# Performance work log

Hardware: AMD Instinct MI355X
Metric: run time of the kernel (lower is better)

## Reference

```python
import jax, jax.numpy as jnp
import numpy as np

N_NODES = 100000
N_EDGES = 1600000
D_IN = 128
D_OUT = 128
EPS = 1e-5


def setup_inputs() -> dict:
    key = jax.random.key(0)
    ks = jax.random.split(key, 5)
    x = jax.random.normal(ks[0], (N_NODES, D_IN), dtype=jnp.float32)
    edge_index = jax.random.randint(ks[1], (2, N_EDGES), 0, N_NODES, dtype=jnp.int64)
    scale = 1.0 / np.sqrt(D_IN)
    W_root = jax.random.normal(ks[2], (D_IN, D_OUT), dtype=jnp.float32) * scale
    W_rel = jax.random.normal(ks[3], (D_IN, D_OUT), dtype=jnp.float32) * scale
    b_rel = jax.random.normal(ks[4], (D_OUT,), dtype=jnp.float32) * 0.01
    gamma = jnp.ones((D_OUT,), dtype=jnp.float32)
    beta = jnp.zeros((D_OUT,), dtype=jnp.float32)
    return {"x": x, "edge_index": edge_index, "W_root": W_root, "W_rel": W_rel,
            "b_rel": b_rel, "gamma": gamma, "beta": beta}


def reference(x, edge_index, W_root, W_rel, b_rel, gamma, beta):
    # GraphConv: out = aggr(x_j) @ W_rel + b_rel + x @ W_root   (aggr = sum)
    src = edge_index[0]
    dst = edge_index[1]
    aggr = jax.ops.segment_sum(x[src], dst, num_segments=x.shape[0])  # [N, D_IN]
    h = aggr @ W_rel + b_rel + x @ W_root                              # [N, D_OUT]
    # NodeLevelBatchNorm (training mode: batch stats over node dim, biased var)
    mean = jnp.mean(h, axis=0)
    var = jnp.mean(jnp.square(h - mean), axis=0)
    h_norm = (h - mean) * jax.lax.rsqrt(var + EPS) * gamma + beta
    return jax.nn.relu(h_norm)
```

## Files before the change

kernel.cpp:

```cpp
#include <hip/hip_runtime.h>

#define N_NODES 100000
#define N_EDGES 1600000
#define D 128
#define NB 196
#define EPT 10
#define CHUNK 2560
#define BIN_BLOCKS 625
#define CVT_X_BLOCKS 6250
#define ZROW N_NODES

typedef __bf16 bf16x8 __attribute__((ext_vector_type(8)));
typedef float f32x4 __attribute__((ext_vector_type(4)));

__device__ __forceinline__ unsigned f2bf(float f) {
    unsigned u = __float_as_uint(f);
    return (u + 0x7fffu + ((u >> 16) & 1u)) >> 16;
}
__device__ __forceinline__ float bf_lo(unsigned u) { return __uint_as_float(u << 16); }
__device__ __forceinline__ float bf_hi(unsigned u) { return __uint_as_float(u & 0xffff0000u); }

__global__ __launch_bounds__(256) void prep_kernel(const float* __restrict__ x,
                                                   const float* __restrict__ Wrel,
                                                   const float* __restrict__ Wroot,
                                                   const int* __restrict__ ei,
                                                   unsigned short* __restrict__ x_bf,
                                                   unsigned short* __restrict__ Wt,
                                                   int* __restrict__ bcount) {
    __shared__ int h[256];
    int b = blockIdx.x;
    int t = threadIdx.x;
    if (b < CVT_X_BLOCKS) {
        size_t i = ((size_t)b * 256 + t) * 8;
        float4 v0 = *(const float4*)(x + i);
        float4 v1 = *(const float4*)(x + i + 4);
        uint4 p;
        p.x = f2bf(v0.x) | (f2bf(v0.y) << 16);
        p.y = f2bf(v0.z) | (f2bf(v0.w) << 16);
        p.z = f2bf(v1.x) | (f2bf(v1.y) << 16);
        p.w = f2bf(v1.z) | (f2bf(v1.w) << 16);
        *(uint4*)(x_bf + i) = p;
    } else if (b < CVT_X_BLOCKS + 128) {
        int c = b - CVT_X_BLOCKS;
        float v = (t < 128) ? Wrel[t * D + c] : Wroot[(t - 128) * D + c];
        Wt[c * 256 + t] = (unsigned short)f2bf(v);
    } else if (b == CVT_X_BLOCKS + 128) {
        if (t < 16) *(uint4*)(x_bf + (size_t)ZROW * D + t * 8) = make_uint4(0, 0, 0, 0);
    } else {
        int blk = b - (CVT_X_BLOCKS + 129);
        h[t] = 0;
        __syncthreads();
        int base = blk * CHUNK;
#pragma unroll
        for (int i = 0; i < EPT; ++i) {
            int dst = ei[N_EDGES + base + i * 256 + t];
            atomicAdd(&h[dst >> 9], 1);
        }
        __syncthreads();
        if (t < NB && h[t]) atomicAdd(&bcount[t], h[t]);
    }
}

__global__ __launch_bounds__(256) void bscan_kernel(const int* __restrict__ bcount,
                                                    int* __restrict__ bucket_base,
                                                    int* __restrict__ bcur) {
    __shared__ int s[256];
    int t = threadIdx.x;
    int v = (t < NB) ? bcount[t] : 0;
    s[t] = v;
    __syncthreads();
    for (int off = 1; off < 256; off <<= 1) {
        int a = (t >= off) ? s[t - off] : 0;
        __syncthreads();
        s[t] += a;
        __syncthreads();
    }
    int excl = s[t] - v;
    if (t < NB) {
        bucket_base[t] = excl;
        bcur[t] = excl;
    }
    if (t == NB) bucket_base[NB] = N_EDGES;
}

__global__ __launch_bounds__(256) void binify_kernel(const int* __restrict__ ei,
                                                     int* __restrict__ bcur,
                                                     unsigned* __restrict__ epk) {
    __shared__ int lhist[256];
    __shared__ int lstart[256];
    __shared__ int lfill[256];
    __shared__ int gbase[256];
    __shared__ uint2 stage[CHUNK];

    int t = threadIdx.x;
    int base = blockIdx.x * CHUNK;
    lhist[t] = 0;
    lfill[t] = 0;
    __syncthreads();

    int src[EPT], dst[EPT];
#pragma unroll
    for (int i = 0; i < EPT; ++i) {
        int e = base + i * 256 + t;
        src[i] = ei[e];
        dst[i] = ei[N_EDGES + e];
        atomicAdd(&lhist[dst[i] >> 9], 1);
    }
    __syncthreads();

    int v = lhist[t];
    lstart[t] = v;
    __syncthreads();
    for (int off = 1; off < 256; off <<= 1) {
        int a = (t >= off) ? lstart[t - off] : 0;
        __syncthreads();
        lstart[t] += a;
        __syncthreads();
    }
    int excl = lstart[t] - v;
    if (t < NB && v > 0) gbase[t] = atomicAdd(&bcur[t], v);
    __syncthreads();
    lstart[t] = excl;
    __syncthreads();

#pragma unroll
    for (int i = 0; i < EPT; ++i) {
        int b = dst[i] >> 9;
        int lp = atomicAdd(&lfill[b], 1);
        stage[lstart[b] + lp] = make_uint2((unsigned)src[i], (unsigned)dst[i]);
    }
    __syncthreads();

    for (int i = t; i < CHUNK; i += 256) {
        uint2 p = stage[i];
        int b = (int)(p.y >> 9);
        unsigned code = p.x | ((p.y & 511u) << 17);
        epk[gbase[b] + (i - lstart[b])] = code;
    }
}

__global__ __launch_bounds__(256) void place_kernel(const unsigned* __restrict__ epk,
                                                    const int* __restrict__ bucket_base,
                                                    int* __restrict__ rowstart,
                                                    int* __restrict__ srcs) {
    __shared__ int bufA[512];
    __shared__ int bufB[512];
    int b = blockIdx.x;
    int t = threadIdx.x;
    int pbeg = bucket_base[b];
    int pend = bucket_base[b + 1];

    bufA[t] = 0;
    bufA[t + 256] = 0;
    __syncthreads();
    for (int i = pbeg + t; i < pend; i += 256)
        atomicAdd(&bufA[epk[i] >> 17], 1);
    __syncthreads();

    for (int j = t; j < 512; j += 256) bufB[j] = j ? bufA[j - 1] : 0;
    __syncthreads();
    int* cur = bufB;
    int* nxt = bufA;
    for (int off = 1; off < 512; off <<= 1) {
        for (int j = t; j < 512; j += 256)
            nxt[j] = cur[j] + ((j >= off) ? cur[j - off] : 0);
        __syncthreads();
        int* tmp = cur; cur = nxt; nxt = tmp;
    }

    for (int j = t; j < 512; j += 256) {
        int gnode = (b << 9) + j;
        int val = pbeg + cur[j];
        if (gnode <= N_NODES) rowstart[gnode] = val;
        nxt[j] = val;
    }
    __syncthreads();

    for (int i = pbeg + t; i < pend; i += 256) {
        unsigned code = epk[i];
        int pos = atomicAdd(&nxt[code >> 17], 1);
        srcs[pos] = (int)(code & 0x1FFFFu);
    }
}

__global__ __launch_bounds__(256) void gather_kernel(const unsigned short* __restrict__ x_bf,
                                                     const int* __restrict__ rowstart,
                                                     const int* __restrict__ srcs,
                                                     unsigned short* __restrict__ aggr_bf) {
    int t = threadIdx.x;
    int node = blockIdx.x * 16 + (t >> 4);
    int l16 = t & 15;
    int begin = rowstart[node];
    int end = rowstart[node + 1];
    const unsigned short* xp = x_bf + l16 * 8;
    float a0 = 0.f, a1 = 0.f, a2 = 0.f, a3 = 0.f;
    float a4 = 0.f, a5 = 0.f, a6 = 0.f, a7 = 0.f;
    for (int e = begin; e < end; e += 8) {
        int idx[8];
#pragma unroll
        for (int i = 0; i < 8; ++i) {
            int ee = e + i;
            int ec = (ee < end) ? ee : (end - 1);
            int sv = srcs[ec];
            idx[i] = (ee < end) ? sv : ZROW;
        }
        uint4 u[8];
#pragma unroll
        for (int i = 0; i < 8; ++i) u[i] = *(const uint4*)(xp + (size_t)idx[i] * D);
#pragma unroll
        for (int i = 0; i < 8; ++i) {
            a0 += bf_lo(u[i].x);
            a1 += bf_hi(u[i].x);
            a2 += bf_lo(u[i].y);
            a3 += bf_hi(u[i].y);
            a4 += bf_lo(u[i].z);
            a5 += bf_hi(u[i].z);
            a6 += bf_lo(u[i].w);
            a7 += bf_hi(u[i].w);
        }
    }
    uint4 w;
    w.x = f2bf(a0) | (f2bf(a1) << 16);
    w.y = f2bf(a2) | (f2bf(a3) << 16);
    w.z = f2bf(a4) | (f2bf(a5) << 16);
    w.w = f2bf(a6) | (f2bf(a7) << 16);
    *(uint4*)(aggr_bf + (size_t)node * D + l16 * 8) = w;
}

#define LDSTRIDE 40
__global__ __launch_bounds__(256) void gemm_mfma(const unsigned short* __restrict__ aggr_bf,
                                                 const unsigned short* __restrict__ x_bf,
                                                 const unsigned short* __restrict__ Wt,
                                                 const float* __restrict__ brel,
                                                 unsigned short* __restrict__ h_bf,
                                                 float* __restrict__ gsum,
                                                 float* __restrict__ gss) {
    __shared__ unsigned short As[128][LDSTRIDE];
    __shared__ unsigned short Bs[128][LDSTRIDE];
    __shared__ float sbias[128];
    __shared__ float SredS[4][128];
    __shared__ float SredQ[4][128];

    const int t = threadIdx.x;
    const int wave = t >> 6;
    const int lane = t & 63;
    const int quad = lane >> 4;
    const int l16 = lane & 15;
    const int blockRow = blockIdx.x * 128;

    if (t < 128) sbias[t] = brel[t];

    f32x4 acc[2][8];
#pragma unroll
    for (int i = 0; i < 2; ++i)
#pragma unroll
        for (int j = 0; j < 8; ++j) acc[i][j] = (f32x4){0.f, 0.f, 0.f, 0.f};

    for (int kc = 0; kc < 8; ++kc) {
        const unsigned short* Asrc = (kc < 4) ? aggr_bf : x_bf;
        const int k0 = (kc & 3) * 32;
#pragma unroll
        for (int s = t; s < 512; s += 256) {
            int row = s >> 2;
            int q = (s & 3) * 8;
            int grow = blockRow + row;
            uint4 v = make_uint4(0, 0, 0, 0);
            if (grow < N_NODES) v = *(const uint4*)(Asrc + (size_t)grow * D + k0 + q);
            *(uint4*)&As[row][q] = v;
        }
#pragma unroll
        for (int s = t; s < 512; s += 256) {
            int col = s >> 2;
            int q = (s & 3) * 8;
            uint4 v = *(const uint4*)(Wt + col * 256 + kc * 32 + q);
            *(uint4*)&Bs[col][q] = v;
        }
        __syncthreads();

        bf16x8 afrag0 = *(bf16x8*)&As[wave * 32 + l16][quad * 8];
        bf16x8 afrag1 = *(bf16x8*)&As[wave * 32 + 16 + l16][quad * 8];
#pragma unroll
        for (int ct = 0; ct < 8; ++ct) {
            bf16x8 bfrag = *(bf16x8*)&Bs[ct * 16 + l16][quad * 8];
            acc[0][ct] = __builtin_amdgcn_mfma_f32_16x16x32_bf16(afrag0, bfrag, acc[0][ct], 0, 0, 0);
            acc[1][ct] = __builtin_amdgcn_mfma_f32_16x16x32_bf16(afrag1, bfrag, acc[1][ct], 0, 0, 0);
        }
        __syncthreads();
    }

    float csum[8], css[8];
#pragma unroll
    for (int ct = 0; ct < 8; ++ct) { csum[ct] = 0.f; css[ct] = 0.f; }

#pragma unroll
    for (int rt = 0; rt < 2; ++rt) {
#pragma unroll
        for (int ct = 0; ct < 8; ++ct) {
            int col = ct * 16 + l16;
            float bv = sbias[col];
#pragma unroll
            for (int reg = 0; reg < 4; ++reg) {
                int row = blockRow + wave * 32 + rt * 16 + quad * 4 + reg;
                if (row < N_NODES) {
                    float v = acc[rt][ct][reg] + bv;
                    h_bf[(size_t)row * D + col] = (unsigned short)f2bf(v);
                    csum[ct] += v;
                    css[ct] += v * v;
                }
            }
        }
    }
#pragma unroll
    for (int ct = 0; ct < 8; ++ct) {
        float s = csum[ct], q = css[ct];
        s += __shfl_xor(s, 16);
        s += __shfl_xor(s, 32);
        q += __shfl_xor(q, 16);
        q += __shfl_xor(q, 32);
        if (quad == 0) {
            SredS[wave][ct * 16 + l16] = s;
            SredQ[wave][ct * 16 + l16] = q;
        }
    }
    __syncthreads();
    if (t < 128) {
        float s = SredS[0][t] + SredS[1][t] + SredS[2][t] + SredS[3][t];
        float q = SredQ[0][t] + SredQ[1][t] + SredQ[2][t] + SredQ[3][t];
        unsafeAtomicAdd(&gsum[t], s);
        unsafeAtomicAdd(&gss[t], q);
    }
}

__global__ __launch_bounds__(256) void norm_kernel(const unsigned short* __restrict__ h_bf,
                                                   float* __restrict__ out,
                                                   const float* __restrict__ gsum,
                                                   const float* __restrict__ gss,
                                                   const float* __restrict__ gamma,
                                                   const float* __restrict__ beta) {
    __shared__ float sscale[128];
    __shared__ float sshift[128];
    int t = threadIdx.x;
    if (t < 128) {
        const float inv_n = 1.0f / (float)N_NODES;
        float mean = gsum[t] * inv_n;
        float var = gss[t] * inv_n - mean * mean;
        float rs = rsqrtf(var + 1e-5f);
        float sc = gamma[t] * rs;
        sscale[t] = sc;
        sshift[t] = beta[t] - mean * sc;
    }
    __syncthreads();
    size_t e = ((size_t)blockIdx.x * 256 + t) * 4;
    if (e >= (size_t)N_NODES * D) return;
    int c = (int)(e & 127);
    uint2 u = *(const uint2*)(h_bf + e);
    float4 v;
    v.x = fmaxf(bf_lo(u.x) * sscale[c + 0] + sshift[c + 0], 0.f);
    v.y = fmaxf(bf_hi(u.x) * sscale[c + 1] + sshift[c + 1], 0.f);
    v.z = fmaxf(bf_lo(u.y) * sscale[c + 2] + sshift[c + 2], 0.f);
    v.w = fmaxf(bf_hi(u.y) * sscale[c + 3] + sshift[c + 3], 0.f);
    *(float4*)(out + e) = v;
}

extern "C" void kernel_launch(void* const* d_in, const int* in_sizes, int n_in,
                              void* d_out, int out_size, void* d_ws, size_t ws_size,
                              hipStream_t stream) {
    const float* x     = (const float*)d_in[0];
    const int*   ei    = (const int*)d_in[1];
    const float* Wroot = (const float*)d_in[2];
    const float* Wrel  = (const float*)d_in[3];
    const float* brel  = (const float*)d_in[4];
    const float* gamma = (const float*)d_in[5];
    const float* beta  = (const float*)d_in[6];
    float* out = (float*)d_out;

    unsigned short* aggr_bf = (unsigned short*)d_ws;
    unsigned short* x_bf    = aggr_bf + (size_t)N_NODES * D;
    unsigned short* Wt      = x_bf + (size_t)(N_NODES + 1) * D;
    float* gsum  = (float*)(Wt + 128 * 256);
    float* gss   = gsum + 128;
    int* bcount  = (int*)(gss + 128);
    int* bucket_base = bcount + 256;
    int* bcur    = bucket_base + 256;
    int* rowstart = bcur + 256;
    unsigned* epk = (unsigned*)(rowstart + 100352);
    int* srcs    = (int*)(epk + N_EDGES);
    unsigned short* h_bf = (unsigned short*)epk;

    hipMemsetAsync(gsum, 0, 512 * sizeof(int), stream);

    prep_kernel<<<CVT_X_BLOCKS + 129 + BIN_BLOCKS, 256, 0, stream>>>(
        x, Wrel, Wroot, ei, x_bf, Wt, bcount);
    bscan_kernel<<<1, 256, 0, stream>>>(bcount, bucket_base, bcur);
    binify_kernel<<<BIN_BLOCKS, 256, 0, stream>>>(ei, bcur, epk);
    place_kernel<<<NB, 256, 0, stream>>>(epk, bucket_base, rowstart, srcs);
    gather_kernel<<<N_NODES / 16, 256, 0, stream>>>(x_bf, rowstart, srcs, aggr_bf);
    gemm_mfma<<<(N_NODES + 127) / 128, 256, 0, stream>>>(aggr_bf, x_bf, Wt, brel, h_bf, gsum, gss);
    norm_kernel<<<12500, 256, 0, stream>>>(h_bf, out, gsum, gss, gamma, beta);
}
```

Measured before the change: 287.8 us.

## Load GEMM A fragments directly from global and stage W in fragment order

The MFMA GEMM no longer stages A tiles through LDS. Each wave reads its bf16x8 A fragments straight from global memory. The weight matrix is copied into LDS once per half (aggregate part, then root part) in MFMA-fragment order, so each lane reads its B fragment contiguously. This cuts the number of block barriers from 16 to 3 and removes the padded-stride LDS traffic for A. In exchange, A loads are no longer coalesced through shared memory, and the row-bounds check on A reads is gone, so the last block reads past N_NODES unless the buffers are padded.

```diff
diff --git a/kernel.cpp b/kernel.cpp
--- a/kernel.cpp
+++ b/kernel.cpp
@@ -227,7 +227,6 @@
     *(uint4*)(aggr_bf + (size_t)node * D + l16 * 8) = w;
 }
 
-#define LDSTRIDE 40
 __global__ __launch_bounds__(256) void gemm_mfma(const unsigned short* __restrict__ aggr_bf,
                                                  const unsigned short* __restrict__ x_bf,
                                                  const unsigned short* __restrict__ Wt,
@@ -235,8 +234,7 @@
                                                  unsigned short* __restrict__ h_bf,
                                                  float* __restrict__ gsum,
                                                  float* __restrict__ gss) {
-    __shared__ unsigned short As[128][LDSTRIDE];
-    __shared__ unsigned short Bs[128][LDSTRIDE];
+    __shared__ unsigned short Bf[2048 * 8];
     __shared__ float sbias[128];
     __shared__ float SredS[4][128];
     __shared__ float SredQ[4][128];
@@ -256,36 +254,35 @@
 #pragma unroll
         for (int j = 0; j < 8; ++j) acc[i][j] = (f32x4){0.f, 0.f, 0.f, 0.f};
 
-    for (int kc = 0; kc < 8; ++kc) {
-        const unsigned short* Asrc = (kc < 4) ? aggr_bf : x_bf;
-        const int k0 = (kc & 3) * 32;
-#pragma unroll
-        for (int s = t; s < 512; s += 256) {
-            int row = s >> 2;
-            int q = (s & 3) * 8;
-            int grow = blockRow + row;
-            uint4 v = make_uint4(0, 0, 0, 0);
-            if (grow < N_NODES) v = *(const uint4*)(Asrc + (size_t)grow * D + k0 + q);
-            *(uint4*)&As[row][q] = v;
-        }
-#pragma unroll
-        for (int s = t; s < 512; s += 256) {
-            int col = s >> 2;
-            int q = (s & 3) * 8;
-            uint4 v = *(const uint4*)(Wt + col * 256 + kc * 32 + q);
-            *(uint4*)&Bs[col][q] = v;
-        }
-        __syncthreads();
-
-        bf16x8 afrag0 = *(bf16x8*)&As[wave * 32 + l16][quad * 8];
-        bf16x8 afrag1 = *(bf16x8*)&As[wave * 32 + 16 + l16][quad * 8];
-#pragma unroll
-        for (int ct = 0; ct < 8; ++ct) {
-            bf16x8 bfrag = *(bf16x8*)&Bs[ct * 16 + l16][quad * 8];
-            acc[0][ct] = __builtin_amdgcn_mfma_f32_16x16x32_bf16(afrag0, bfrag, acc[0][ct], 0, 0, 0);
-            acc[1][ct] = __builtin_amdgcn_mfma_f32_16x16x32_bf16(afrag1, bfrag, acc[1][ct], 0, 0, 0);
-        }
-        __syncthreads();
+    const int rowb = blockRow + wave * 32;
+
+#pragma unroll
+    for (int half = 0; half < 2; ++half) {
+#pragma unroll
+        for (int f = t; f < 2048; f += 256) {
+            int kcl = f >> 9;
+            int ct = (f >> 6) & 7;
+            int ln = f & 63;
+            int col = ct * 16 + (ln & 15);
+            int kb = half * 128 + kcl * 32 + ((ln >> 4) << 3);
+            *(uint4*)&Bf[f * 8] = *(const uint4*)(Wt + col * 256 + kb);
+        }
+        __syncthreads();
+
+        const unsigned short* Asrc = half ? x_bf : aggr_bf;
+#pragma unroll
+        for (int kcl = 0; kcl < 4; ++kcl) {
+            const int k0 = kcl * 32 + quad * 8;
+            bf16x8 af0 = *(const bf16x8*)(Asrc + (size_t)(rowb + l16) * D + k0);
+            bf16x8 af1 = *(const bf16x8*)(Asrc + (size_t)(rowb + 16 + l16) * D + k0);
+#pragma unroll
+            for (int ct = 0; ct < 8; ++ct) {
+                bf16x8 bfrag = *(const bf16x8*)&Bf[((kcl * 8 + ct) * 64 + lane) * 8];
+                acc[0][ct] = __builtin_amdgcn_mfma_f32_16x16x32_bf16(af0, bfrag, acc[0][ct], 0, 0, 0);
+                acc[1][ct] = __builtin_amdgcn_mfma_f32_16x16x32_bf16(af1, bfrag, acc[1][ct], 0, 0, 0);
+            }
+        }
+        if (half == 0) __syncthreads();
     }
 
     float csum[8], css[8];
```

Result: no change. 282.9 us (-1.7%).
